# Kernel optimization log

Measured on AMD Instinct MI355X. Metric: run time of the kernel, lower is better.

Reference implementation:

```python
import jax, jax.numpy as jnp
import numpy as np

N_EMBD = 1024
N_HEAD = 16
HEAD_DIM = N_EMBD // N_HEAD
BLOCK = 2048
BATCH = 2


def setup_inputs() -> dict:
    key = jax.random.key(0)
    ks = jax.random.split(key, 6)
    s_in = 1.0 / np.sqrt(N_EMBD)
    s_hd = 1.0 / np.sqrt(N_EMBD)  # fan-in of c_proj1 is n_head*head_dim = n_embd
    return {
        "x": jax.random.normal(ks[0], (BATCH, BLOCK, N_EMBD), jnp.float32),
        "wq": jax.random.normal(ks[1], (N_EMBD, N_HEAD, HEAD_DIM), jnp.float32) * s_in,
        "wk": jax.random.normal(ks[2], (N_EMBD, N_HEAD, HEAD_DIM), jnp.float32) * s_in,
        "wv": jax.random.normal(ks[3], (N_EMBD, N_HEAD, HEAD_DIM), jnp.float32) * s_in,
        "wp1": jax.random.normal(ks[4], (N_HEAD, HEAD_DIM, N_EMBD), jnp.float32) * s_hd,
        "wp2": jax.random.normal(ks[5], (N_EMBD, N_EMBD), jnp.float32) * s_in,
    }


def reference(x, wq, wk, wv, wp1, wp2):
    # QKV projections: DenseGeneral(features=(H, D), axis=-1), no bias
    q = jnp.einsum('btc,chd->bthd', x, wq)
    k = jnp.einsum('btc,chd->bthd', x, wk)
    v = jnp.einsum('btc,chd->bthd', x, wv)
    scale = HEAD_DIM ** (-0.5)
    wei = jnp.einsum('bqhd,bkhd->bhqk', q, k) * scale  # [B,H,T,T]
    tril = jnp.tril(jnp.ones((BLOCK, BLOCK), dtype=bool))
    wei = jnp.where(tril, wei, -jnp.inf)
    wei = jax.nn.softmax(wei, axis=-1)
    att = jnp.einsum('bhqk,bkhd->bqhd', wei, v)  # [B,T,H,D]
    # c_proj1: DenseGeneral over (-2,-1) -> contract (H,D)
    y = jnp.einsum('bqhd,hdc->bqc', att, wp1)
    # c_proj2: Dense
    out = jnp.einsum('bqc,ce->bqe', y, wp2)
    return out
```

## Files before the change

### kernel.cpp

```cpp
#include <hip/hip_runtime.h>
#include <hip/hip_bf16.h>
#include <stdint.h>

typedef __bf16 bf16;
typedef __bf16 bf16x4 __attribute__((ext_vector_type(4)));
typedef __bf16 bf16x8 __attribute__((ext_vector_type(8)));
typedef float  f32x4  __attribute__((ext_vector_type(4)));

#define MFMA16(a,b,c) __builtin_amdgcn_mfma_f32_16x16x32_bf16((a),(b),(c),0,0,0)

#define TSEQ 2048
#define NE   1024
#define NE3  3072
#define NH   16
#define HD   64
#define MTOK 4096

#if defined(__has_builtin) && __has_builtin(__builtin_amdgcn_exp2f)
#define EXP2F(x) __builtin_amdgcn_exp2f(x)
#else
__device__ __forceinline__ float exp2_fast(float x) {
  float r; asm("v_exp_f32 %0, %1" : "=v"(r) : "v"(x)); return r;
}
#define EXP2F(x) exp2_fast(x)
#endif

__device__ __forceinline__ void gl_lds16(const bf16* g, bf16* l) {
  __builtin_amdgcn_global_load_lds(
      (const __attribute__((address_space(1))) void*)g,
      (__attribute__((address_space(3))) void*)l,
      16, 0, 0);
}

__global__ void k_cast(const float* __restrict__ in, bf16* __restrict__ out, int n4) {
  int i = blockIdx.x * blockDim.x + threadIdx.x;
  if (i < n4) {
    float4 v = reinterpret_cast<const float4*>(in)[i];
    bf16x4 o = { (bf16)v.x, (bf16)v.y, (bf16)v.z, (bf16)v.w };
    reinterpret_cast<bf16x4*>(out)[i] = o;
  }
}

__global__ void k_transpose_all(const float* __restrict__ wq, const float* __restrict__ wk,
                                const float* __restrict__ wv, const float* __restrict__ wp2,
                                const float* __restrict__ wp1,
                                bf16* __restrict__ W3T, bf16* __restrict__ Wp2T,
                                bf16* __restrict__ Wp1b) {
  __shared__ float tile[64][65];
  const int z = blockIdx.z;
  const int r0 = blockIdx.y * 64, c0 = blockIdx.x * 64;
  const int lc = threadIdx.x & 63, lr0 = threadIdx.x >> 6;
  if (z == 4) {
#pragma unroll
    for (int i = 0; i < 16; ++i) {
      int lr = i*4 + lr0;
      Wp1b[(size_t)(r0 + lr)*1024 + c0 + lc] = (bf16)wp1[(size_t)(r0 + lr)*1024 + c0 + lc];
    }
    return;
  }
  const float* in = (z == 0) ? wq : (z == 1) ? wk : (z == 2) ? wv : wp2;
  bf16* out = (z < 3) ? (W3T + (size_t)z * 1024 * 1024) : Wp2T;
#pragma unroll
  for (int i = 0; i < 16; ++i) {
    int lr = i*4 + lr0;
    tile[lr][lc] = in[(size_t)(r0 + lr) * 1024 + (c0 + lc)];
  }
  __syncthreads();
#pragma unroll
  for (int i = 0; i < 16; ++i) {
    int lr = i*4 + lr0;
    out[(size_t)(c0 + lr) * 1024 + (r0 + lc)] = (bf16)tile[lc][lr];
  }
}

__global__ void k_transpose_v(const bf16* __restrict__ V, bf16* __restrict__ Vt) {
  __shared__ bf16 tile[64][65];
  const int b = blockIdx.z, h = blockIdx.y, t0 = blockIdx.x * 64;
  const int lc = threadIdx.x & 63, lr0 = threadIdx.x >> 6;
#pragma unroll
  for (int i = 0; i < 16; ++i) {
    int lr = i*4 + lr0;
    tile[lr][lc] = V[(size_t)(b*TSEQ + t0 + lr)*NE3 + h*HD + lc];
  }
  __syncthreads();
#pragma unroll
  for (int i = 0; i < 16; ++i) {
    int lr = i*4 + lr0;
    Vt[((size_t)(b*NH + h)*HD + lr)*TSEQ + t0 + lc] = tile[lc][lr];
  }
}

template<int BN, typename OutT>
__global__ __launch_bounds__(256) void k_gemm_bt(const bf16* __restrict__ A,
                                                 const bf16* __restrict__ Bt,
                                                 OutT* __restrict__ C,
                                                 const int M, const int N, const int K) {
  constexpr int NC = BN / 32;
  __shared__ bf16 As[2][128*32];
  __shared__ bf16 Bs[2][BN*32];
  const int tid  = threadIdx.x;
  const int lane = tid & 63;
  const int wave = tid >> 6;
  const int wr = (wave >> 1) * 64;
  const int wc = (wave & 1) * (BN/2);
  const int l15 = lane & 15;
  const int l4  = lane >> 4;

  const int nwg = gridDim.x * gridDim.y;
  int id = blockIdx.y * gridDim.x + blockIdx.x;
  id = (id & 7) * (nwg >> 3) + (id >> 3);
  const int bm = (id / gridDim.x) * 128;
  const int bn = (id % gridDim.x) * BN;

  const int srow = tid >> 2;
  const int scol = ((tid & 3) ^ ((tid >> 3) & 3)) * 8;
  const bf16* ag = A  + (size_t)(bm + srow) * K + scol;
  const bf16* bg = Bt + (size_t)(bn + srow) * K + scol;
  const int kx = (l4 ^ ((l15 >> 1) & 3)) * 8;

  f32x4 acc[4][NC] = {};

  auto stage = [&](int buf, int k0) {
    bf16* al = As[buf] + tid * 8;
    bf16* bl = Bs[buf] + tid * 8;
    gl_lds16(ag + k0,                   al);
    gl_lds16(ag + k0 + (size_t)64 * K,  al + 64*32);
    gl_lds16(bg + k0,                   bl);
    if (BN == 128) gl_lds16(bg + k0 + (size_t)64 * K, bl + 64*32);
  };

  stage(0, 0);
  __syncthreads();
  int cur = 0;
  for (int k0 = 0; k0 < K; k0 += 32) {
    if (k0 + 32 < K) stage(cur ^ 1, k0 + 32);
    bf16x8 af[4], bfr[NC];
#pragma unroll
    for (int m = 0; m < 4; ++m)
      af[m] = *reinterpret_cast<const bf16x8*>(&As[cur][(wr + m*16 + l15)*32 + kx]);
#pragma unroll
    for (int n = 0; n < NC; ++n)
      bfr[n] = *reinterpret_cast<const bf16x8*>(&Bs[cur][(wc + n*16 + l15)*32 + kx]);
#pragma unroll
    for (int m = 0; m < 4; ++m)
#pragma unroll
      for (int n = 0; n < NC; ++n)
        acc[m][n] = MFMA16(af[m], bfr[n], acc[m][n]);
    __syncthreads();
    cur ^= 1;
  }

#pragma unroll
  for (int m = 0; m < 4; ++m) {
    const int row = bm + wr + m*16 + l4*4;
#pragma unroll
    for (int n = 0; n < NC; ++n) {
      const int col = bn + wc + n*16 + l15;
#pragma unroll
      for (int r = 0; r < 4; ++r)
        C[(size_t)(row + r) * N + col] = (OutT)acc[m][n][r];
    }
  }
}

__global__ __launch_bounds__(512) void k_attn(const bf16* __restrict__ QKV,
                                              const bf16* __restrict__ Vt,
                                              bf16* __restrict__ O) {
  __shared__ bf16 Ks[2][2*128*32];
  __shared__ bf16 Vs[2][4*64*32];
  __shared__ bf16 Ps[8][4*16*32];

  const int tid  = threadIdx.x;
  const int lane = tid & 63;
  const int wave = tid >> 6;
  const int l15 = lane & 15;
  const int l4  = lane >> 4;

  const int x  = blockIdx.x;
  const int p  = x >> 5;
  const int bh = x & 31;
  const int b  = bh >> 4, h = bh & 15;

  const bf16* Qb = QKV + (size_t)b*TSEQ*NE3 +        h*HD;
  const bf16* Kb = QKV + (size_t)b*TSEQ*NE3 + 1024 + h*HD;
  const bf16* Vb = Vt  + (size_t)bh*HD*TSEQ;
  bf16* Pw = Ps[wave];

  const float SC = 0.125f * 1.44269504f;
  const int swz = (l4 ^ ((l15 >> 1) & 3)) * 8;
  const int key = (l15 >> 1) & 3;

  const int krow = tid >> 2;
  const int kg   = (tid & 3) ^ ((krow >> 1) & 3);
  const int vd   = (tid >> 2) & 63;
  const int vg   = (tid & 3) ^ ((vd >> 1) & 3);
  const int vp0  = tid >> 8;

  auto stage = [&](int buf, int t) {
#pragma unroll
    for (int kk = 0; kk < 2; ++kk)
      gl_lds16(&Kb[(size_t)(t*128 + krow)*NE3 + kk*32 + kg*8],
               &Ks[buf][kk*4096 + tid*8]);
#pragma unroll
    for (int kk = 0; kk < 2; ++kk) {
      const int ksv = kk*2 + vp0;
      gl_lds16(&Vb[(size_t)vd*TSEQ + t*128 + ksv*32 + vg*8],
               &Vs[buf][kk*4096 + tid*8]);
    }
  };

  stage(0, 0);
  __syncthreads();
  int cur = 0;
  int i = 0;

  for (int ci = 0; ci < 2; ++ci) {
    const int c  = ci ? (15 - p) : p;
    const int qw = c*128 + wave*16;

    bf16x8 qf[2];
#pragma unroll
    for (int ks = 0; ks < 2; ++ks) {
      bf16x8 qv = *reinterpret_cast<const bf16x8*>(
          &Qb[(size_t)(qw + l15)*NE3 + ks*32 + l4*8]);
#pragma unroll
      for (int j = 0; j < 8; ++j) qv[j] = (bf16)((float)qv[j] * SC);
      qf[ks] = qv;
    }

    f32x4 ot[4] = {};
    float m_run = -1e30f;
    float l_part = 0.f;

    for (int t = 0; t <= c; ++t, ++i) {
      if (i + 1 < 17) {
        const int nxt = (i + 1 <= p) ? (i + 1) : (i - p);
        stage(cur ^ 1, nxt);
      }

      f32x4 st[8];
#pragma unroll
      for (int kvf = 0; kvf < 8; ++kvf) {
        st[kvf] = f32x4{0.f, 0.f, 0.f, 0.f};
        const int row = kvf*16 + l15;
#pragma unroll
        for (int ks = 0; ks < 2; ++ks) {
          bf16x8 kf = *reinterpret_cast<const bf16x8*>(&Ks[cur][ks*4096 + row*32 + swz]);
          st[kvf] = MFMA16(kf, qf[ks], st[kvf]);
        }
      }

      if (t == c) {
#pragma unroll
        for (int kvf = 0; kvf < 8; ++kvf)
#pragma unroll
          for (int r = 0; r < 4; ++r)
            if (kvf*16 + l4*4 + r > wave*16 + l15) st[kvf][r] = -1e30f;
      }

      float mx = st[0][0];
#pragma unroll
      for (int kvf = 0; kvf < 8; ++kvf)
#pragma unroll
        for (int r = 0; r < 4; ++r) mx = fmaxf(mx, st[kvf][r]);
      mx = fmaxf(mx, __shfl_xor(mx, 16));
      mx = fmaxf(mx, __shfl_xor(mx, 32));

      if (__any(mx > m_run + 8.f)) {
        const float mnew = fmaxf(m_run, mx);
        const float corr = EXP2F(m_run - mnew);
        l_part *= corr;
#pragma unroll
        for (int n2 = 0; n2 < 4; ++n2) ot[n2] *= corr;
        m_run = mnew;
      }

      float rs = 0.f;
#pragma unroll
      for (int kvf = 0; kvf < 8; ++kvf) {
        bf16x4 pk;
#pragma unroll
        for (int r = 0; r < 4; ++r) {
          const float pv = EXP2F(st[kvf][r] - m_run);
          rs += pv;
          pk[r] = (bf16)pv;
        }
        const int gp = (((kvf & 1)*2 + (l4 >> 1)) ^ key);
        *reinterpret_cast<bf16x4*>(
            &Pw[(kvf>>1)*512 + l15*32 + gp*8 + (l4 & 1)*4]) = pk;
      }
      l_part += rs;

      bf16x8 pa[4];
#pragma unroll
      for (int ksv = 0; ksv < 4; ++ksv)
        pa[ksv] = *reinterpret_cast<const bf16x8*>(&Pw[ksv*512 + l15*32 + swz]);
#pragma unroll
      for (int n2 = 0; n2 < 4; ++n2) {
        const int vrow = n2*16 + l15;
#pragma unroll
        for (int ksv = 0; ksv < 4; ++ksv) {
          bf16x8 vf = *reinterpret_cast<const bf16x8*>(&Vs[cur][ksv*2048 + vrow*32 + swz]);
          ot[n2] = MFMA16(vf, pa[ksv], ot[n2]);
        }
      }

      __syncthreads();
      cur ^= 1;
    }

    float l = l_part;
    l += __shfl_xor(l, 16);
    l += __shfl_xor(l, 32);
    const float rl = 1.f / l;
    const size_t row = (size_t)(b*TSEQ + qw + l15);
#pragma unroll
    for (int n2 = 0; n2 < 4; ++n2) {
      bf16x4 ov;
#pragma unroll
      for (int r = 0; r < 4; ++r) ov[r] = (bf16)(ot[n2][r] * rl);
      *reinterpret_cast<bf16x4*>(&O[row*NE + h*HD + n2*16 + l4*4]) = ov;
    }
  }
}

extern "C" void kernel_launch(void* const* d_in, const int* in_sizes, int n_in,
                              void* d_out, int out_size, void* d_ws, size_t ws_size,
                              hipStream_t stream) {
  const float* x   = (const float*)d_in[0];
  const float* wq  = (const float*)d_in[1];
  const float* wk  = (const float*)d_in[2];
  const float* wv  = (const float*)d_in[3];
  const float* wp1 = (const float*)d_in[4];
  const float* wp2 = (const float*)d_in[5];
  float* out = (float*)d_out;

  char* ws = (char*)d_ws;
  const size_t MB = 1024ull * 1024ull;
  bf16* xb   = (bf16*)(ws + 0*MB);
  bf16* W3T  = (bf16*)(ws + 8*MB);
  bf16* wp1b = (bf16*)(ws + 14*MB);
  bf16* wp2T = (bf16*)(ws + 16*MB);
  bf16* WcT  = (bf16*)(ws + 18*MB);
  bf16* QKVb = (bf16*)(ws + 20*MB);
  bf16* Vtb  = (bf16*)(ws + 44*MB);
  bf16* attb = (bf16*)(ws + 52*MB);

  k_cast<<<4096, 256, 0, stream>>>(x, xb, MTOK*NE/4);
  k_transpose_all<<<dim3(16, 16, 5), 256, 0, stream>>>(wq, wk, wv, wp2, wp1,
                                                       W3T, wp2T, wp1b);

  k_gemm_bt<64, bf16><<<dim3(16, 8), 256, 0, stream>>>(wp2T, wp1b, WcT, 1024, 1024, 1024);

  k_gemm_bt<128, bf16><<<dim3(24, 32), 256, 0, stream>>>(xb, W3T, QKVb, MTOK, NE3, NE);

  k_transpose_v<<<dim3(TSEQ/64, NH, 2), 256, 0, stream>>>(QKVb + 2048, Vtb);

  k_attn<<<dim3(256), 512, 0, stream>>>(QKVb, Vtb, attb);

  k_gemm_bt<128, float><<<dim3(8, 32), 256, 0, stream>>>(attb, WcT, out, MTOK, NE, NE);
}
```

Measured before the change: 128.4 us.

## Triple-buffer K/V tiles in attention with two-ahead prefetch and partial vmcnt wait

Replaces the double-buffered K/V shared-memory staging with a three-slot ring and prefetches two tiles ahead. Each iteration waits only on the older loads via a partial vmcnt wait and uses a single barrier at the top instead of a trailing __syncthreads. This is meant to hide more global-load latency behind the MFMA work and to drop one barrier per iteration. In exchange it uses more LDS, which may lower occupancy, and it relies on hand-written waitcnt and sched_barrier ordering being correct.

```diff
diff --git a/kernel.cpp b/kernel.cpp
--- a/kernel.cpp
+++ b/kernel.cpp
@@ -166,8 +166,7 @@
 __global__ __launch_bounds__(512) void k_attn(const bf16* __restrict__ QKV,
                                               const bf16* __restrict__ Vt,
                                               bf16* __restrict__ O) {
-  __shared__ bf16 Ks[2][2*128*32];
-  __shared__ bf16 Vs[2][4*64*32];
+  __shared__ bf16 KVs[3][16384];
   __shared__ bf16 Ps[8][4*16*32];
 
   const int tid  = threadIdx.x;
@@ -196,22 +195,23 @@
   const int vg   = (tid & 3) ^ ((vd >> 1) & 3);
   const int vp0  = tid >> 8;
 
+  auto tileOf = [&](int j) { return (j <= p) ? j : (j - p - 1); };
+
   auto stage = [&](int buf, int t) {
+    bf16* kb = &KVs[buf][0];
+    bf16* vb = &KVs[buf][8192];
 #pragma unroll
     for (int kk = 0; kk < 2; ++kk)
-      gl_lds16(&Kb[(size_t)(t*128 + krow)*NE3 + kk*32 + kg*8],
-               &Ks[buf][kk*4096 + tid*8]);
+      gl_lds16(&Kb[(size_t)(t*128 + krow)*NE3 + kk*32 + kg*8], kb + kk*4096 + tid*8);
 #pragma unroll
     for (int kk = 0; kk < 2; ++kk) {
       const int ksv = kk*2 + vp0;
-      gl_lds16(&Vb[(size_t)vd*TSEQ + t*128 + ksv*32 + vg*8],
-               &Vs[buf][kk*4096 + tid*8]);
+      gl_lds16(&Vb[(size_t)vd*TSEQ + t*128 + ksv*32 + vg*8],  vb + kk*4096 + tid*8);
     }
   };
 
-  stage(0, 0);
-  __syncthreads();
-  int cur = 0;
+  stage(0, tileOf(0));
+  stage(1, tileOf(1));
   int i = 0;
 
   for (int ci = 0; ci < 2; ++ci) {
@@ -233,10 +233,16 @@
     float l_part = 0.f;
 
     for (int t = 0; t <= c; ++t, ++i) {
-      if (i + 1 < 17) {
-        const int nxt = (i + 1 <= p) ? (i + 1) : (i - p);
-        stage(cur ^ 1, nxt);
-      }
+      asm volatile("s_waitcnt vmcnt(4)" ::: "memory");
+      __builtin_amdgcn_sched_barrier(0);
+      __builtin_amdgcn_s_barrier();
+      __builtin_amdgcn_sched_barrier(0);
+      const int j2 = (i + 2 <= 16) ? (i + 2) : 16;
+      stage((i + 2) % 3, tileOf(j2));
+      __builtin_amdgcn_sched_barrier(0);
+
+      const bf16* kbuf = &KVs[i % 3][0];
+      const bf16* vbuf = &KVs[i % 3][8192];
 
       f32x4 st[8];
 #pragma unroll
@@ -245,7 +251,7 @@
         const int row = kvf*16 + l15;
 #pragma unroll
         for (int ks = 0; ks < 2; ++ks) {
-          bf16x8 kf = *reinterpret_cast<const bf16x8*>(&Ks[cur][ks*4096 + row*32 + swz]);
+          bf16x8 kf = *reinterpret_cast<const bf16x8*>(&kbuf[ks*4096 + row*32 + swz]);
           st[kvf] = MFMA16(kf, qf[ks], st[kvf]);
         }
       }
@@ -300,13 +306,10 @@
         const int vrow = n2*16 + l15;
 #pragma unroll
         for (int ksv = 0; ksv < 4; ++ksv) {
-          bf16x8 vf = *reinterpret_cast<const bf16x8*>(&Vs[cur][ksv*2048 + vrow*32 + swz]);
+          bf16x8 vf = *reinterpret_cast<const bf16x8*>(&vbuf[ksv*2048 + vrow*32 + swz]);
           ot[n2] = MFMA16(vf, pa[ksv], ot[n2]);
         }
       }
-
-      __syncthreads();
-      cur ^= 1;
     }
 
     float l = l_part;
```

Measured after the change: 129.5 us. Within noise of the previous version (+0.9%).

## Fuse V transpose into QKV GEMM epilogue and raise MFMA wave priority

Applied to the files above, without the earlier changes.

The QKV projection GEMM now writes the V columns straight into the transposed per-head Vt layout from its epilogue, using packed bf16x4 stores along the token dimension. This removes the separate transpose kernel launch and its extra read and write of V. The attention kernel also wraps its QK and PV MFMA blocks in s_setprio so those waves get issue priority over waves doing softmax or loads. V is no longer stored in QKVb, which is fine since attention reads V only from Vt.

```diff
diff --git a/kernel.cpp b/kernel.cpp
--- a/kernel.cpp
+++ b/kernel.cpp
@@ -73,27 +73,11 @@
   }
 }
 
-__global__ void k_transpose_v(const bf16* __restrict__ V, bf16* __restrict__ Vt) {
-  __shared__ bf16 tile[64][65];
-  const int b = blockIdx.z, h = blockIdx.y, t0 = blockIdx.x * 64;
-  const int lc = threadIdx.x & 63, lr0 = threadIdx.x >> 6;
-#pragma unroll
-  for (int i = 0; i < 16; ++i) {
-    int lr = i*4 + lr0;
-    tile[lr][lc] = V[(size_t)(b*TSEQ + t0 + lr)*NE3 + h*HD + lc];
-  }
-  __syncthreads();
-#pragma unroll
-  for (int i = 0; i < 16; ++i) {
-    int lr = i*4 + lr0;
-    Vt[((size_t)(b*NH + h)*HD + lr)*TSEQ + t0 + lc] = tile[lc][lr];
-  }
-}
-
-template<int BN, typename OutT>
+template<int BN, typename OutT, bool VTF>
 __global__ __launch_bounds__(256) void k_gemm_bt(const bf16* __restrict__ A,
                                                  const bf16* __restrict__ Bt,
                                                  OutT* __restrict__ C,
+                                                 bf16* __restrict__ VtOut,
                                                  const int M, const int N, const int K) {
   constexpr int NC = BN / 32;
   __shared__ bf16 As[2][128*32];
@@ -150,15 +134,33 @@
     cur ^= 1;
   }
 
-#pragma unroll
-  for (int m = 0; m < 4; ++m) {
-    const int row = bm + wr + m*16 + l4*4;
-#pragma unroll
-    for (int n = 0; n < NC; ++n) {
-      const int col = bn + wc + n*16 + l15;
-#pragma unroll
-      for (int r = 0; r < 4; ++r)
-        C[(size_t)(row + r) * N + col] = (OutT)acc[m][n][r];
+  if (VTF && bn >= 2048) {
+    const int bB  = bm >> 11;
+    const int tb0 = (bm & 2047) + wr + l4*4;
+#pragma unroll
+    for (int m = 0; m < 4; ++m) {
+      const int tb = tb0 + m*16;
+#pragma unroll
+      for (int n = 0; n < NC; ++n) {
+        const int dg = (bn - 2048) + wc + n*16 + l15;
+        bf16x4 ov;
+#pragma unroll
+        for (int r = 0; r < 4; ++r) ov[r] = (bf16)acc[m][n][r];
+        *reinterpret_cast<bf16x4*>(
+            &VtOut[((size_t)(bB*16 + (dg >> 6))*64 + (dg & 63))*2048 + tb]) = ov;
+      }
+    }
+  } else {
+#pragma unroll
+    for (int m = 0; m < 4; ++m) {
+      const int row = bm + wr + m*16 + l4*4;
+#pragma unroll
+      for (int n = 0; n < NC; ++n) {
+        const int col = bn + wc + n*16 + l15;
+#pragma unroll
+        for (int r = 0; r < 4; ++r)
+          C[(size_t)(row + r) * N + col] = (OutT)acc[m][n][r];
+      }
     }
   }
 }
@@ -238,6 +240,7 @@
         stage(cur ^ 1, nxt);
       }
 
+      __builtin_amdgcn_s_setprio(1);
       f32x4 st[8];
 #pragma unroll
       for (int kvf = 0; kvf < 8; ++kvf) {
@@ -249,6 +252,7 @@
           st[kvf] = MFMA16(kf, qf[ks], st[kvf]);
         }
       }
+      __builtin_amdgcn_s_setprio(0);
 
       if (t == c) {
 #pragma unroll
@@ -295,6 +299,7 @@
 #pragma unroll
       for (int ksv = 0; ksv < 4; ++ksv)
         pa[ksv] = *reinterpret_cast<const bf16x8*>(&Pw[ksv*512 + l15*32 + swz]);
+      __builtin_amdgcn_s_setprio(1);
 #pragma unroll
       for (int n2 = 0; n2 < 4; ++n2) {
         const int vrow = n2*16 + l15;
@@ -304,6 +309,7 @@
           ot[n2] = MFMA16(vf, pa[ksv], ot[n2]);
         }
       }
+      __builtin_amdgcn_s_setprio(0);
 
       __syncthreads();
       cur ^= 1;
@@ -350,13 +356,14 @@
   k_transpose_all<<<dim3(16, 16, 5), 256, 0, stream>>>(wq, wk, wv, wp2, wp1,
                                                        W3T, wp2T, wp1b);
 
-  k_gemm_bt<64, bf16><<<dim3(16, 8), 256, 0, stream>>>(wp2T, wp1b, WcT, 1024, 1024, 1024);
-
-  k_gemm_bt<128, bf16><<<dim3(24, 32), 256, 0, stream>>>(xb, W3T, QKVb, MTOK, NE3, NE);
-
-  k_transpose_v<<<dim3(TSEQ/64, NH, 2), 256, 0, stream>>>(QKVb + 2048, Vtb);
+  k_gemm_bt<64, bf16, false><<<dim3(16, 8), 256, 0, stream>>>(
+      wp2T, wp1b, WcT, nullptr, 1024, 1024, 1024);
+
+  k_gemm_bt<128, bf16, true><<<dim3(24, 32), 256, 0, stream>>>(
+      xb, W3T, QKVb, Vtb, MTOK, NE3, NE);
 
   k_attn<<<dim3(256), 512, 0, stream>>>(QKVb, Vtb, attb);
 
-  k_gemm_bt<128, float><<<dim3(8, 32), 256, 0, stream>>>(attb, WcT, out, MTOK, NE, NE);
-}
+  k_gemm_bt<128, float, false><<<dim3(8, 32), 256, 0, stream>>>(
+      attb, WcT, out, nullptr, MTOK, NE, NE);
+}
```

After: 125.4 us. 1.02x faster.
